# Performance work log

Measured on AMD Instinct MI355X. Metric: run time of the kernel, lower is better.

Reference implementation:

```python
import jax, jax.numpy as jnp
import numpy as np

# Constants from GaussianSplattingCompliance.__init__
SCALE_MIN, SCALE_MAX = 0.05, 1.5
RATIO_MIN, RATIO_MAX = 0.5, 3.5
ROT_MIN, ROT_MAX = -np.pi / 2, np.pi / 2
AXIS_OFFSET = 0.05
EMIN = 1e-9
SMOOTH_K = 10.0

N_POINTS = 131072  # number of FE element centers (512x256 mesh, flattened)
N_G = 256          # number of gaussians (args['args']['N_g'])


def setup_inputs() -> dict:
    key = jax.random.key(0)
    k0, k1, k2, k3, k4 = jax.random.split(key, 5)
    coords = jax.random.uniform(k0, (N_POINTS, 2), dtype=jnp.float32)
    W_scale = jax.random.normal(k1, (N_G, 1), dtype=jnp.float32)
    W_shape_var = jax.random.normal(k2, (N_G, 1), dtype=jnp.float32)
    W_rotation = jax.random.normal(k3, (N_G, 1), dtype=jnp.float32)
    W_offsets = jax.random.normal(k4, (N_G, 2), dtype=jnp.float32)
    return {"coords": coords, "W_scale": W_scale, "W_shape_var": W_shape_var,
            "W_rotation": W_rotation, "W_offsets": W_offsets}


def reference(coords, W_scale, W_shape_var, W_rotation, W_offsets):
    # coord bounds are constant buffers in the original module (computed once in __init__)
    c = jax.lax.stop_gradient(coords)
    cmin, cmax = c.min(axis=0), c.max(axis=0)                      # (2,)
    coord_min = cmin - cmax * AXIS_OFFSET
    coord_max = cmax + cmax * AXIS_OFFSET

    B = W_scale.shape[0]
    base_scale = (SCALE_MAX - SCALE_MIN) * jax.nn.sigmoid(W_scale)[:, 0] + SCALE_MIN   # (B,)
    ratio = (RATIO_MAX - RATIO_MIN) * jax.nn.sigmoid(W_shape_var) + RATIO_MIN          # (B,1)
    sigmas = jnp.concatenate([jnp.ones((B, 1), coords.dtype), ratio], axis=1)          # (B,2)
    rotation = ROT_MIN + (ROT_MAX - ROT_MIN) * jax.nn.sigmoid(W_rotation)[:, 0]        # (B,)
    offsets = coord_min + (coord_max - coord_min) * jax.nn.sigmoid(W_offsets)          # (B,2)

    cos_r, sin_r = jnp.cos(rotation), jnp.sin(rotation)
    R = jnp.stack([jnp.stack([cos_r, -sin_r], axis=-1),
                   jnp.stack([sin_r, cos_r], axis=-1)], axis=-2)                       # (B,2,2)
    inv_cov_diag = 1.0 / (sigmas ** 2 + 1e-6)                                          # (B,2)

    # (B, N, 2): centered, scaled coordinates per gaussian
    xy = (coords[None, :, :] - offsets[:, None, :]) / (base_scale[:, None, None] + 1e-8)
    rxy = jnp.einsum('bij,bnj->bni', R, xy)                                            # (B,N,2)
    # diagonal Mahalanobis quadratic form
    z = jnp.sqrt(jnp.einsum('bni,bi,bni->bn', rxy, inv_cov_diag, rxy))                 # (B,N)
    kernel = jax.nn.sigmoid(-10.0 * (z - 1.0))                                         # 1/(1+exp(10(z-1)))
    kernel_sum = kernel.sum(axis=0) + 1e-8                                             # (N,)
    H = (1.0 - EMIN) * jax.nn.sigmoid(-SMOOTH_K * (kernel_sum - 0.5)) + EMIN           # (N,)
    return H
```

## Files before the change

### kernel.cpp

```cpp
#include <hip/hip_runtime.h>
#include <cmath>

#define N_GAUSS 256

__global__ __launch_bounds__(256) void k_partial_minmax(
    const float2* __restrict__ coords, int n, float4* __restrict__ partial) {
  int tid = blockIdx.x * blockDim.x + threadIdx.x;
  int stride = gridDim.x * blockDim.x;
  float mnx = INFINITY, mny = INFINITY, mxx = -INFINITY, mxy = -INFINITY;
  for (int i = tid; i < n; i += stride) {
    float2 c = coords[i];
    mnx = fminf(mnx, c.x);
    mny = fminf(mny, c.y);
    mxx = fmaxf(mxx, c.x);
    mxy = fmaxf(mxy, c.y);
  }
  for (int o = 32; o > 0; o >>= 1) {
    mnx = fminf(mnx, __shfl_down(mnx, o));
    mny = fminf(mny, __shfl_down(mny, o));
    mxx = fmaxf(mxx, __shfl_down(mxx, o));
    mxy = fmaxf(mxy, __shfl_down(mxy, o));
  }
  __shared__ float4 lds[4];
  if ((threadIdx.x & 63) == 0) lds[threadIdx.x >> 6] = make_float4(mnx, mny, mxx, mxy);
  __syncthreads();
  if (threadIdx.x == 0) {
    float4 r = lds[0];
    for (int w = 1; w < 4; ++w) {
      float4 o = lds[w];
      r.x = fminf(r.x, o.x);
      r.y = fminf(r.y, o.y);
      r.z = fmaxf(r.z, o.z);
      r.w = fmaxf(r.w, o.w);
    }
    partial[blockIdx.x] = r;
  }
}

__global__ __launch_bounds__(256) void k_params(
    const float4* __restrict__ partial,
    const float* __restrict__ W_scale,
    const float* __restrict__ W_shape_var,
    const float* __restrict__ W_rotation,
    const float* __restrict__ W_offsets,
    float4* __restrict__ params) {
  int t = threadIdx.x;
  float4 r = partial[t];
  for (int o = 32; o > 0; o >>= 1) {
    r.x = fminf(r.x, __shfl_down(r.x, o));
    r.y = fminf(r.y, __shfl_down(r.y, o));
    r.z = fmaxf(r.z, __shfl_down(r.z, o));
    r.w = fmaxf(r.w, __shfl_down(r.w, o));
  }
  __shared__ float4 lds[4];
  __shared__ float4 bounds;
  if ((t & 63) == 0) lds[t >> 6] = r;
  __syncthreads();
  if (t == 0) {
    float4 a = lds[0];
    for (int w = 1; w < 4; ++w) {
      float4 o = lds[w];
      a.x = fminf(a.x, o.x);
      a.y = fminf(a.y, o.y);
      a.z = fmaxf(a.z, o.z);
      a.w = fmaxf(a.w, o.w);
    }
    bounds = a;
  }
  __syncthreads();
  float4 c = bounds;

  double cminx = (double)c.x, cminy = (double)c.y;
  double cmaxx = (double)c.z, cmaxy = (double)c.w;
  double cmin0 = cminx - cmaxx * 0.05;
  double cmin1 = cminy - cmaxy * 0.05;
  double cmax0 = cmaxx + cmaxx * 0.05;
  double cmax1 = cmaxy + cmaxy * 0.05;

  double sS = 1.0 / (1.0 + exp(-(double)W_scale[t]));
  double base_scale = (1.5 - 0.05) * sS + 0.05;
  double sV = 1.0 / (1.0 + exp(-(double)W_shape_var[t]));
  double ratio = (3.5 - 0.5) * sV + 0.5;
  double sR = 1.0 / (1.0 + exp(-(double)W_rotation[t]));
  const double PI = 3.14159265358979323846;
  double rot = -PI * 0.5 + PI * sR;
  double sOx = 1.0 / (1.0 + exp(-(double)W_offsets[2 * t]));
  double sOy = 1.0 / (1.0 + exp(-(double)W_offsets[2 * t + 1]));
  double ox = cmin0 + (cmax0 - cmin0) * sOx;
  double oy = cmin1 + (cmax1 - cmin1) * sOy;

  double cr = cos(rot), sr = sin(rot);
  double inv_s = 1.0 / (base_scale + 1e-8);
  double r0 = sqrt(1.0 / (1.0 + 1e-6));
  double r1 = sqrt(1.0 / (ratio * ratio + 1e-6));

  double A = r0 * cr * inv_s;
  double B = -r0 * sr * inv_s;
  double E = -(A * ox + B * oy);
  double C = r1 * sr * inv_s;
  double D = r1 * cr * inv_s;
  double F = -(C * ox + D * oy);

  params[2 * t]     = make_float4((float)A, (float)B, (float)E, (float)C);
  params[2 * t + 1] = make_float4((float)D, (float)F, 0.0f, 0.0f);
}

__global__ __launch_bounds__(256) void k_main(
    const float2* __restrict__ coords,
    const float4* __restrict__ params,
    float* __restrict__ out, int n) {
  __shared__ float4 sp[2 * N_GAUSS];
  sp[threadIdx.x] = params[threadIdx.x];
  sp[threadIdx.x + 256] = params[threadIdx.x + 256];
  __syncthreads();

  int i = blockIdx.x * blockDim.x + threadIdx.x;
  if (i >= n) return;
  float2 c = coords[i];
  float x = c.x, y = c.y;
  float ks = 1e-8f;
  const float K1 = 14.4269504088896339f;

  for (int b0 = 0; b0 < N_GAUSS; b0 += 8) {
#pragma unroll
    for (int j = 0; j < 8; ++j) {
      int b = b0 + j;
      float4 p0 = sp[2 * b];
      float4 p1 = sp[2 * b + 1];
      float u = fmaf(p0.x, x, fmaf(p0.y, y, p0.z));
      float v = fmaf(p0.w, x, fmaf(p1.x, y, p1.y));
      float z = sqrtf(fmaf(u, u, v * v));
      float t = __builtin_amdgcn_exp2f(fmaf(K1, z, -K1));
      ks += __builtin_amdgcn_rcpf(1.0f + t);
    }
    if (__all(ks > 6.0f)) break;
  }

  float t2 = __builtin_amdgcn_exp2f(fmaf(K1, ks, -0.5f * K1));
  float s = __builtin_amdgcn_rcpf(1.0f + t2);
  out[i] = fmaf(1e-9f, 1.0f - s, s);
}

extern "C" void kernel_launch(void* const* d_in, const int* in_sizes, int n_in,
                              void* d_out, int out_size, void* d_ws, size_t ws_size,
                              hipStream_t stream) {
  const float* coords      = (const float*)d_in[0];
  const float* W_scale     = (const float*)d_in[1];
  const float* W_shape_var = (const float*)d_in[2];
  const float* W_rotation  = (const float*)d_in[3];
  const float* W_offsets   = (const float*)d_in[4];
  float* out = (float*)d_out;

  int n = in_sizes[0] / 2;

  float4* partial = (float4*)d_ws;
  float4* params  = (float4*)((char*)d_ws + 4096);

  k_partial_minmax<<<256, 256, 0, stream>>>((const float2*)coords, n, partial);
  k_params<<<1, 256, 0, stream>>>(partial, W_scale, W_shape_var, W_rotation,
                                  W_offsets, params);
  int blocks = (n + 255) / 256;
  k_main<<<blocks, 256, 0, stream>>>((const float2*)coords, params, out, n);
}
```

Baseline: 68.03 us.

## Fuse gaussian parameter computation into main kernel and switch it to float

Removes the single-block k_params launch. Every block of the main kernel now reduces the min/max partials itself and computes all 256 gaussian parameter sets directly into LDS. The double-precision math is replaced with fast float sigmoid, sinf/cosf and rsqrtf. This drops one kernel launch and its serial dependency, but every one of the 512 blocks now repeats the reduction and parameter math, and float precision could shift results slightly.

```diff
diff --git a/kernel.cpp b/kernel.cpp
--- a/kernel.cpp
+++ b/kernel.cpp
@@ -37,14 +37,25 @@
   }
 }
 
-__global__ __launch_bounds__(256) void k_params(
+__device__ __forceinline__ float sigmoidf_fast(float w) {
+  float t = __builtin_amdgcn_exp2f(-1.4426950408889634f * w);
+  return 1.0f / (1.0f + t);
+}
+
+__global__ __launch_bounds__(256) void k_fused_main(
+    const float2* __restrict__ coords,
     const float4* __restrict__ partial,
     const float* __restrict__ W_scale,
     const float* __restrict__ W_shape_var,
     const float* __restrict__ W_rotation,
     const float* __restrict__ W_offsets,
-    float4* __restrict__ params) {
+    float* __restrict__ out, int n) {
+  __shared__ float4 sp[2 * N_GAUSS];
+  __shared__ float4 lds4[4];
+  __shared__ float4 boundsS;
+
   int t = threadIdx.x;
+
   float4 r = partial[t];
   for (int o = 32; o > 0; o >>= 1) {
     r.x = fminf(r.x, __shfl_down(r.x, o));
@@ -52,66 +63,55 @@
     r.z = fmaxf(r.z, __shfl_down(r.z, o));
     r.w = fmaxf(r.w, __shfl_down(r.w, o));
   }
-  __shared__ float4 lds[4];
-  __shared__ float4 bounds;
-  if ((t & 63) == 0) lds[t >> 6] = r;
+  if ((t & 63) == 0) lds4[t >> 6] = r;
   __syncthreads();
   if (t == 0) {
-    float4 a = lds[0];
+    float4 a = lds4[0];
     for (int w = 1; w < 4; ++w) {
-      float4 o = lds[w];
+      float4 o = lds4[w];
       a.x = fminf(a.x, o.x);
       a.y = fminf(a.y, o.y);
       a.z = fmaxf(a.z, o.z);
       a.w = fmaxf(a.w, o.w);
     }
-    bounds = a;
+    boundsS = a;
   }
   __syncthreads();
-  float4 c = bounds;
+  float4 bc = boundsS;
 
-  double cminx = (double)c.x, cminy = (double)c.y;
-  double cmaxx = (double)c.z, cmaxy = (double)c.w;
-  double cmin0 = cminx - cmaxx * 0.05;
-  double cmin1 = cminy - cmaxy * 0.05;
-  double cmax0 = cmaxx + cmaxx * 0.05;
-  double cmax1 = cmaxy + cmaxy * 0.05;
+  {
+    float cmin0 = bc.x - bc.z * 0.05f;
+    float cmin1 = bc.y - bc.w * 0.05f;
+    float cmax0 = bc.z + bc.z * 0.05f;
+    float cmax1 = bc.w + bc.w * 0.05f;
 
-  double sS = 1.0 / (1.0 + exp(-(double)W_scale[t]));
-  double base_scale = (1.5 - 0.05) * sS + 0.05;
-  double sV = 1.0 / (1.0 + exp(-(double)W_shape_var[t]));
-  double ratio = (3.5 - 0.5) * sV + 0.5;
-  double sR = 1.0 / (1.0 + exp(-(double)W_rotation[t]));
-  const double PI = 3.14159265358979323846;
-  double rot = -PI * 0.5 + PI * sR;
-  double sOx = 1.0 / (1.0 + exp(-(double)W_offsets[2 * t]));
-  double sOy = 1.0 / (1.0 + exp(-(double)W_offsets[2 * t + 1]));
-  double ox = cmin0 + (cmax0 - cmin0) * sOx;
-  double oy = cmin1 + (cmax1 - cmin1) * sOy;
+    float sS = sigmoidf_fast(W_scale[t]);
+    float base_scale = 1.45f * sS + 0.05f;
+    float sV = sigmoidf_fast(W_shape_var[t]);
+    float ratio = 3.0f * sV + 0.5f;
+    float sR = sigmoidf_fast(W_rotation[t]);
+    const float PIf = 3.14159265358979323846f;
+    float rot = -0.5f * PIf + PIf * sR;
+    float sOx = sigmoidf_fast(W_offsets[2 * t]);
+    float sOy = sigmoidf_fast(W_offsets[2 * t + 1]);
+    float ox = cmin0 + (cmax0 - cmin0) * sOx;
+    float oy = cmin1 + (cmax1 - cmin1) * sOy;
 
-  double cr = cos(rot), sr = sin(rot);
-  double inv_s = 1.0 / (base_scale + 1e-8);
-  double r0 = sqrt(1.0 / (1.0 + 1e-6));
-  double r1 = sqrt(1.0 / (ratio * ratio + 1e-6));
+    float cr = cosf(rot), sr = sinf(rot);
+    float inv_s = 1.0f / (base_scale + 1e-8f);
+    float r0 = rsqrtf(1.0f + 1e-6f);
+    float r1 = rsqrtf(fmaf(ratio, ratio, 1e-6f));
 
-  double A = r0 * cr * inv_s;
-  double B = -r0 * sr * inv_s;
-  double E = -(A * ox + B * oy);
-  double C = r1 * sr * inv_s;
-  double D = r1 * cr * inv_s;
-  double F = -(C * ox + D * oy);
+    float A = r0 * cr * inv_s;
+    float B = -r0 * sr * inv_s;
+    float E = -fmaf(A, ox, B * oy);
+    float C = r1 * sr * inv_s;
+    float D = r1 * cr * inv_s;
+    float F = -fmaf(C, ox, D * oy);
 
-  params[2 * t]     = make_float4((float)A, (float)B, (float)E, (float)C);
-  params[2 * t + 1] = make_float4((float)D, (float)F, 0.0f, 0.0f);
-}
-
-__global__ __launch_bounds__(256) void k_main(
-    const float2* __restrict__ coords,
-    const float4* __restrict__ params,
-    float* __restrict__ out, int n) {
-  __shared__ float4 sp[2 * N_GAUSS];
-  sp[threadIdx.x] = params[threadIdx.x];
-  sp[threadIdx.x + 256] = params[threadIdx.x + 256];
+    sp[2 * t]     = make_float4(A, B, E, C);
+    sp[2 * t + 1] = make_float4(D, F, 0.0f, 0.0f);
+  }
   __syncthreads();
 
   int i = blockIdx.x * blockDim.x + threadIdx.x;
@@ -130,8 +130,8 @@
       float u = fmaf(p0.x, x, fmaf(p0.y, y, p0.z));
       float v = fmaf(p0.w, x, fmaf(p1.x, y, p1.y));
       float z = sqrtf(fmaf(u, u, v * v));
-      float t = __builtin_amdgcn_exp2f(fmaf(K1, z, -K1));
-      ks += __builtin_amdgcn_rcpf(1.0f + t);
+      float tt = __builtin_amdgcn_exp2f(fmaf(K1, z, -K1));
+      ks += __builtin_amdgcn_rcpf(1.0f + tt);
     }
     if (__all(ks > 6.0f)) break;
   }
@@ -154,11 +154,10 @@
   int n = in_sizes[0] / 2;
 
   float4* partial = (float4*)d_ws;
-  float4* params  = (float4*)((char*)d_ws + 4096);
 
   k_partial_minmax<<<256, 256, 0, stream>>>((const float2*)coords, n, partial);
-  k_params<<<1, 256, 0, stream>>>(partial, W_scale, W_shape_var, W_rotation,
-                                  W_offsets, params);
   int blocks = (n + 255) / 256;
-  k_main<<<blocks, 256, 0, stream>>>((const float2*)coords, params, out, n);
+  k_fused_main<<<blocks, 256, 0, stream>>>((const float2*)coords, partial,
+                                           W_scale, W_shape_var, W_rotation,
+                                           W_offsets, out, n);
 }
```

After: 66.85 us. No clear change (-1.7%).
